# Optimization experiments

Measured on AMD Instinct MI355X. Metric: run time of the kernel, lower is better.

## Reference

```python
import jax, jax.numpy as jnp
import numpy as np

H = W = 32
CROP = int(H * 0.8)  # 25, matches int(H*crop_ratio) in torch
MEAN = jnp.array([0.5071, 0.4867, 0.4408], jnp.float32).reshape(1, 3, 1, 1)
STD = jnp.array([0.2675, 0.2565, 0.2761], jnp.float32).reshape(1, 3, 1, 1)


def _bilinear(img, iy, ix):
    # img [C,H,W]; iy/ix [H,W] float pixel coords (reflected+clamped already)
    y0 = jnp.floor(iy); x0 = jnp.floor(ix)
    wy = iy - y0; wx = ix - x0
    y0i = jnp.clip(y0.astype(jnp.int32), 0, H - 1); y1i = jnp.clip(y0i + 1, 0, H - 1)
    x0i = jnp.clip(x0.astype(jnp.int32), 0, W - 1); x1i = jnp.clip(x0i + 1, 0, W - 1)
    v00 = img[:, y0i, x0i]; v01 = img[:, y0i, x1i]
    v10 = img[:, y1i, x0i]; v11 = img[:, y1i, x1i]
    return v00 * (1 - wy) * (1 - wx) + v01 * (1 - wy) * wx + v10 * wy * (1 - wx) + v11 * wy * wx


def _reflect(c, size):
    # PyTorch grid_sample reflection padding, align_corners=False (reflect about -0.5 / size-0.5)
    lo = -0.5
    span = float(size)
    t = jnp.abs(c - lo)
    extra = jnp.mod(t, span)
    flips = jnp.floor(t / span)
    out = jnp.where(jnp.mod(flips, 2.0) == 0.0, lo + extra, lo + span - extra)
    return jnp.clip(out, 0.0, size - 1.0)


def _crop_resize_one(img, top, left):
    # bilinear resize of img[:, top:top+CROP, left:left+CROP] -> HxW, align_corners=False
    d = (jnp.arange(W, dtype=jnp.float32) + 0.5) * (CROP / W) - 0.5
    d = jnp.maximum(d, 0.0)
    i0 = jnp.floor(d).astype(jnp.int32)
    lam = d - i0
    i1 = jnp.minimum(i0 + 1, CROP - 1)
    r0 = top + i0; r1 = top + i1; c0 = left + i0; c1 = left + i1
    v00 = img[:, r0[:, None], c0[None, :]]
    v01 = img[:, r0[:, None], c1[None, :]]
    v10 = img[:, r1[:, None], c0[None, :]]
    v11 = img[:, r1[:, None], c1[None, :]]
    ly = lam[:, None]; lx = lam[None, :]
    return v00 * (1 - ly) * (1 - lx) + v01 * (1 - ly) * lx + v10 * ly * (1 - lx) + v11 * ly * lx


def _grid_sample_one(img, theta):
    # affine_grid + grid_sample (bilinear, reflection, align_corners=False)
    xs = (2.0 * (jnp.arange(W, dtype=jnp.float32) + 0.5) / W) - 1.0
    ys = (2.0 * (jnp.arange(H, dtype=jnp.float32) + 0.5) / H) - 1.0
    yn, xn = jnp.meshgrid(ys, xs, indexing='ij')
    gx = theta[0, 0] * xn + theta[0, 1] * yn + theta[0, 2]
    gy = theta[1, 0] * xn + theta[1, 1] * yn + theta[1, 2]
    ix = _reflect(((gx + 1.0) * W - 1.0) * 0.5, W)
    iy = _reflect(((gy + 1.0) * H - 1.0) * 0.5, H)
    return _bilinear(img, iy, ix)


def _augment(x, shared_affine, apply_crop):
    B = x.shape[0]
    ks = jax.random.split(jax.random.key(42), 10)
    x = x * STD + MEAN  # de-normalize
    if apply_crop:
        max_off = H - CROP
        top = jax.random.randint(ks[0], (B,), 0, max_off + 1)
        left = jax.random.randint(ks[1], (B,), 0, max_off + 1)
        x = jax.vmap(_crop_resize_one)(x, top, left)
    flip_mask = jax.random.uniform(ks[2], (B,)) < 0.5
    x = jnp.where(flip_mask[:, None, None, None], x[..., ::-1], x)
    # shared affine is provided -> always applied (torch shared_affine branch)
    x = jax.vmap(_grid_sample_one)(x, shared_affine)
    brightness = 1.0 + (jax.random.uniform(ks[3], (B, 1, 1, 1)) - 0.5) * 0.8
    x = x * brightness
    gray = x.mean(axis=1, keepdims=True)
    contrast = 1.0 + (jax.random.uniform(ks[4], (B, 1, 1, 1)) - 0.5) * 0.8
    x = gray + (x - gray) * contrast
    gray = x.mean(axis=1, keepdims=True)
    saturation = 1.0 + (jax.random.uniform(ks[5], (B, 1, 1, 1)) - 0.5) * 0.8
    x = gray + (x - gray) * saturation
    hue_mask = jax.random.uniform(ks[6], (B,)) < 0.5
    x = jnp.where(hue_mask[:, None, None, None], x[:, ::-1], x)  # BGR swap
    gray_mask = jax.random.uniform(ks[7], (B,)) < 0.2
    x = jnp.where(gray_mask[:, None, None, None], x.mean(axis=1, keepdims=True), x)
    blur_mask = jax.random.uniform(ks[8], (B,)) < 0.5
    xp = jnp.pad(x, ((0, 0), (0, 0), (1, 1), (1, 1)), mode='edge')  # replicate pad
    bl = sum(xp[:, :, i:i + H, j:j + W] for i in range(3) for j in range(3)) / 9.0  # 3x3 box blur
    x = jnp.where(blur_mask[:, None, None, None], bl, x)
    solar_mask = jax.random.uniform(ks[9], (B,)) < 0.1
    x = jnp.where(solar_mask[:, None, None, None] & (x > 0.5), 1.0 - x, x)
    x = jnp.clip(x, 0.0, 1.0)
    x = (x - MEAN) / STD  # re-normalize
    return x, flip_mask


def setup_inputs() -> dict:
    key = jax.random.key(0)
    k1, k2 = jax.random.split(key)
    B = 8192
    x = jax.random.normal(k1, (B, 3, H, W), jnp.float32)
    eye = jnp.broadcast_to(jnp.array([[1.0, 0.0, 0.0], [0.0, 1.0, 0.0]], jnp.float32), (B, 2, 3))
    shared_affine = eye + 0.1 * jax.random.normal(k2, (B, 2, 3), jnp.float32)
    return {"x": x, "shared_affine": shared_affine, "apply_crop": 1}


def reference(x, shared_affine, apply_crop):
    out, flip_mask = _augment(x, shared_affine, int(apply_crop))
    # torch returns (x, {'flip': flip_mask, 'affine': affine_theta})
    return out, flip_mask, shared_affine
```

## Files before the change

### kernel.cpp

```cpp
#include <hip/hip_runtime.h>

#define HW 32
#define NPIX 1024
#define IMG 3072

__device__ __forceinline__ unsigned rotl32(unsigned x, int d) {
    return (x << d) | (x >> (32 - d));
}

struct UPair { unsigned a, b; };

__device__ __forceinline__ UPair threefry2x32(unsigned k0, unsigned k1,
                                              unsigned x0, unsigned x1) {
    unsigned k2 = k0 ^ k1 ^ 0x1BD11BDAu;
    x0 += k0; x1 += k1;
#define RND(r) { x0 += x1; x1 = rotl32(x1, (r)); x1 ^= x0; }
    RND(13) RND(15) RND(26) RND(6)
    x0 += k1; x1 += k2 + 1u;
    RND(17) RND(29) RND(16) RND(24)
    x0 += k2; x1 += k0 + 2u;
    RND(13) RND(15) RND(26) RND(6)
    x0 += k0; x1 += k1 + 3u;
    RND(17) RND(29) RND(16) RND(24)
    x0 += k1; x1 += k2 + 4u;
    RND(13) RND(15) RND(26) RND(6)
    x0 += k2; x1 += k0 + 5u;
#undef RND
    return {x0, x1};
}

__device__ __forceinline__ float bits_to_u01(unsigned bits) {
    return __uint_as_float((bits >> 9) | 0x3f800000u) - 1.0f;
}

__device__ __forceinline__ float reflect32(float c) {
    float t = fabsf(c + 0.5f);
    float flips = floorf(t * 0.03125f);
    float extra = fmaf(flips, -32.0f, t);
    float o = (((int)flips) & 1) ? (31.5f - extra) : (extra - 0.5f);
    return fminf(fmaxf(o, 0.0f), 31.0f);
}

__global__ __launch_bounds__(256) void aug_kernel(
    const float* __restrict__ xin, const float* __restrict__ aff,
    const int* __restrict__ apply_crop, float* __restrict__ out, int B) {
    __shared__ __align__(16) float bufA[IMG];
    __shared__ __align__(16) float bufB[IMG];
    __shared__ float s_theta[6];
    __shared__ int s_j0[32];
    __shared__ float s_fr[32];
    __shared__ int s_top, s_left, s_flip, s_hue, s_gray, s_blur, s_solar;
    __shared__ float s_bright, s_contr, s_sat;

    const int b = blockIdx.x;
    const int t = threadIdx.x;
    const bool do_crop = (apply_crop[0] != 0);

    const float MEANc[3] = {0.5071f, 0.4867f, 0.4408f};
    const float STDc[3]  = {0.2675f, 0.2565f, 0.2761f};
    const float INVSTD[3] = {1.0f / 0.2675f, 1.0f / 0.2565f, 1.0f / 0.2761f};

    const float4* imgv = (const float4*)(xin + (size_t)b * IMG);
    float4 ld0 = imgv[t];
    float4 ld1 = imgv[t + 256];
    float4 ld2 = imgv[t + 512];

    const size_t OUT_IMG = (size_t)B * IMG;
    if (t < 6) {
        float v = aff[b * 6 + t];
        s_theta[t] = v;
        out[OUT_IMG + (size_t)B + (size_t)b * 6 + t] = v;
    }

    if (t < 32) {
        float d = fmaxf(((float)t + 0.5f) * 0.78125f - 0.5f, 0.0f);
        int j0 = (int)d;
        s_j0[t] = j0;
        s_fr[t] = d - (float)j0;
    }

    if (t < 10) {
        int k = t;
        UPair K = threefry2x32(0u, 42u, 0u, (unsigned)k);
        if (k < 2) {
            UPair k2 = threefry2x32(K.a, K.b, 0u, 1u);
            UPair r = threefry2x32(k2.a, k2.b, 0u, (unsigned)b);
            int val = (int)((r.a ^ r.b) & 7u);
            if (k == 0) s_top = val; else s_left = val;
        } else {
            UPair r = threefry2x32(K.a, K.b, 0u, (unsigned)b);
            float u = bits_to_u01(r.a ^ r.b);
            if      (k == 2) s_flip  = (u < 0.5f);
            else if (k == 3) s_bright = 1.0f + (u - 0.5f) * 0.8f;
            else if (k == 4) s_contr  = 1.0f + (u - 0.5f) * 0.8f;
            else if (k == 5) s_sat    = 1.0f + (u - 0.5f) * 0.8f;
            else if (k == 6) s_hue   = (u < 0.5f);
            else if (k == 7) s_gray  = (u < 0.2f);
            else if (k == 8) s_blur  = (u < 0.5f);
            else             s_solar = (u < 0.1f);
        }
    }

    {
        float4 v = ld0;
        v.x = v.x * STDc[0] + MEANc[0]; v.y = v.y * STDc[0] + MEANc[0];
        v.z = v.z * STDc[0] + MEANc[0]; v.w = v.w * STDc[0] + MEANc[0];
        ((float4*)bufA)[t] = v;
        v = ld1;
        v.x = v.x * STDc[1] + MEANc[1]; v.y = v.y * STDc[1] + MEANc[1];
        v.z = v.z * STDc[1] + MEANc[1]; v.w = v.w * STDc[1] + MEANc[1];
        ((float4*)bufA)[t + 256] = v;
        v = ld2;
        v.x = v.x * STDc[2] + MEANc[2]; v.y = v.y * STDc[2] + MEANc[2];
        v.z = v.z * STDc[2] + MEANc[2]; v.w = v.w * STDc[2] + MEANc[2];
        ((float4*)bufA)[t + 512] = v;
    }
    __syncthreads();

    if (t == 0) out[OUT_IMG + b] = s_flip ? 1.0f : 0.0f;

    float* cur = bufA;
    float* nxt = bufB;

    if (do_crop) {
        const int top = s_top, left = s_left;
#pragma unroll
        for (int m = 0; m < 4; ++m) {
            int s = t + 256 * m;
            int yi = s >> 5, xj = s & 31;
            int i0 = s_j0[yi]; float ly = s_fr[yi];
            int q0 = s_j0[xj]; float lx = s_fr[xj];
            int i1 = min(i0 + 1, 24);
            int q1 = min(q0 + 1, 24);
            int r0 = (top + i0) << 5, r1 = (top + i1) << 5;
            int c0 = left + q0, c1 = left + q1;
            float omy = 1.0f - ly, omx = 1.0f - lx;
            float w00 = omy * omx, w01 = omy * lx;
            float w10 = ly * omx, w11 = ly * lx;
            int a00 = r0 + c0, a01 = r0 + c1, a10 = r1 + c0, a11 = r1 + c1;
#pragma unroll
            for (int c = 0; c < 3; ++c) {
                const float* p = cur + c * NPIX;
                nxt[c * NPIX + s] = fmaf(p[a00], w00, fmaf(p[a01], w01,
                                    fmaf(p[a10], w10, p[a11] * w11)));
            }
        }
        float* tp = cur; cur = nxt; nxt = tp;
        __syncthreads();
    }

    {
        const int flip = s_flip, hue = s_hue, grayf = s_gray;
        const float br = s_bright;
        const float ctsa = s_contr * s_sat;
        const float th0 = s_theta[0], th1 = s_theta[1], th2 = s_theta[2];
        const float th3 = s_theta[3], th4 = s_theta[4], th5 = s_theta[5];
#pragma unroll
        for (int m = 0; m < 4; ++m) {
            int s = t + 256 * m;
            int yi = s >> 5, xj = s & 31;
            float xn = (float)xj * 0.0625f - 0.96875f;
            float yn = (float)yi * 0.0625f - 0.96875f;
            float gx = fmaf(th0, xn, fmaf(th1, yn, th2));
            float gy = fmaf(th3, xn, fmaf(th4, yn, th5));
            float ix = reflect32(fmaf(gx, 16.0f, 15.5f));
            float iy = reflect32(fmaf(gy, 16.0f, 15.5f));
            float fy = floorf(iy), fx = floorf(ix);
            float wy = iy - fy, wx = ix - fx;
            int y0 = (int)fy; int y1 = min(y0 + 1, 31);
            int x0 = (int)fx; int x1 = min(x0 + 1, 31);
            if (flip) { x0 = 31 - x0; x1 = 31 - x1; }
            int r0 = y0 << 5, r1 = y1 << 5;
            float omy = 1.0f - wy, omx = 1.0f - wx;
            float w00 = omy * omx, w01 = omy * wx;
            float w10 = wy * omx, w11 = wy * wx;
            int a00 = r0 + x0, a01 = r0 + x1, a10 = r1 + x0, a11 = r1 + x1;
            float ch0, ch1, ch2;
            {
                const float* p = cur;
                ch0 = fmaf(p[a00], w00, fmaf(p[a01], w01,
                       fmaf(p[a10], w10, p[a11] * w11)));
            }
            {
                const float* p = cur + NPIX;
                ch1 = fmaf(p[a00], w00, fmaf(p[a01], w01,
                       fmaf(p[a10], w10, p[a11] * w11)));
            }
            {
                const float* p = cur + 2 * NPIX;
                ch2 = fmaf(p[a00], w00, fmaf(p[a01], w01,
                       fmaf(p[a10], w10, p[a11] * w11)));
            }
            ch0 *= br; ch1 *= br; ch2 *= br;
            float g = (ch0 + ch1 + ch2) * (1.0f / 3.0f);
            ch0 = fmaf(ch0 - g, ctsa, g);
            ch1 = fmaf(ch1 - g, ctsa, g);
            ch2 = fmaf(ch2 - g, ctsa, g);
            if (hue) { float tmp = ch0; ch0 = ch2; ch2 = tmp; }
            if (grayf) { ch0 = ch1 = ch2 = g; }
            nxt[s] = ch0; nxt[NPIX + s] = ch1; nxt[2 * NPIX + s] = ch2;
        }
        float* tp = cur; cur = nxt; nxt = tp;
        __syncthreads();
    }

    const int blur = s_blur, solar = s_solar;

    if (blur) {
#pragma unroll
        for (int m = 0; m < 4; ++m) {
            int s = t + 256 * m;
            int yi = s >> 5, xj = s & 31;
            int yc = yi << 5;
            int xm = max(xj - 1, 0), xp = min(xj + 1, 31);
#pragma unroll
            for (int c = 0; c < 3; ++c) {
                const float* p = cur + c * NPIX;
                nxt[c * NPIX + s] = p[yc + xm] + p[yc + xj] + p[yc + xp];
            }
        }
        __syncthreads();
    }

    {
        float* o = out + (size_t)b * IMG;
#pragma unroll
        for (int m = 0; m < 4; ++m) {
            int s = t + 256 * m;
            int yi = s >> 5, xj = s & 31;
            int ym = max(yi - 1, 0) << 5, yp = min(yi + 1, 31) << 5;
#pragma unroll
            for (int c = 0; c < 3; ++c) {
                float r;
                if (blur) {
                    const float* h = nxt + c * NPIX;
                    r = (h[ym + xj] + h[s] + h[yp + xj]) * (1.0f / 9.0f);
                } else {
                    r = cur[c * NPIX + s];
                }
                if (solar && r > 0.5f) r = 1.0f - r;
                r = fminf(fmaxf(r, 0.0f), 1.0f);
                r = (r - MEANc[c]) * INVSTD[c];
                o[c * NPIX + s] = r;
            }
        }
    }
}

extern "C" void kernel_launch(void* const* d_in, const int* in_sizes, int n_in,
                              void* d_out, int out_size, void* d_ws, size_t ws_size,
                              hipStream_t stream) {
    const float* x = (const float*)d_in[0];
    const float* aff = (const float*)d_in[1];
    const int* ac = (const int*)d_in[2];
    float* out = (float*)d_out;
    int B = in_sizes[0] / IMG;
    aug_kernel<<<dim3(B), dim3(256), 0, stream>>>(x, aff, ac, out, B);
}
```

Before: 181.7 us.

## Process each image with one wavefront using interleaved RGB LDS and register pipeline

The kernel now uses one 64-thread wavefront per image instead of 256 threads. Each lane keeps 16 pixels in registers across stages. Shared memory holds a single interleaved RGBx float4 buffer, so each bilinear tap is one vector LDS read, and the double buffer and all block barriers are gone. The horizontal blur uses cross-lane shuffles, per-image parameters are made wave-uniform with readfirstlane, and output stores are float4. The trade-off is fewer waves per CU, which means less latency hiding, and higher register pressure.

```diff
diff --git a/kernel.cpp b/kernel.cpp
--- a/kernel.cpp
+++ b/kernel.cpp
@@ -3,6 +3,8 @@
 #define HW 32
 #define NPIX 1024
 #define IMG 3072
+
+typedef float vf4 __attribute__((ext_vector_type(4)));
 
 __device__ __forceinline__ unsigned rotl32(unsigned x, int d) {
     return (x << d) | (x >> (32 - d));
@@ -41,14 +43,18 @@
     return fminf(fmaxf(o, 0.0f), 31.0f);
 }
 
-__global__ __launch_bounds__(256) void aug_kernel(
+__device__ __forceinline__ float rfl_f(float v) {
+    return __uint_as_float(__builtin_amdgcn_readfirstlane(__float_as_uint(v)));
+}
+__device__ __forceinline__ int rfl_i(int v) {
+    return __builtin_amdgcn_readfirstlane(v);
+}
+
+__global__ __launch_bounds__(64) void aug_kernel(
     const float* __restrict__ xin, const float* __restrict__ aff,
     const int* __restrict__ apply_crop, float* __restrict__ out, int B) {
-    __shared__ __align__(16) float bufA[IMG];
-    __shared__ __align__(16) float bufB[IMG];
+    __shared__ vf4 buf[NPIX];
     __shared__ float s_theta[6];
-    __shared__ int s_j0[32];
-    __shared__ float s_fr[32];
     __shared__ int s_top, s_left, s_flip, s_hue, s_gray, s_blur, s_solar;
     __shared__ float s_bright, s_contr, s_sat;
 
@@ -56,27 +62,21 @@
     const int t = threadIdx.x;
     const bool do_crop = (apply_crop[0] != 0);
 
-    const float MEANc[3] = {0.5071f, 0.4867f, 0.4408f};
-    const float STDc[3]  = {0.2675f, 0.2565f, 0.2761f};
-    const float INVSTD[3] = {1.0f / 0.2675f, 1.0f / 0.2565f, 1.0f / 0.2761f};
-
-    const float4* imgv = (const float4*)(xin + (size_t)b * IMG);
-    float4 ld0 = imgv[t];
-    float4 ld1 = imgv[t + 256];
-    float4 ld2 = imgv[t + 512];
+    const float* src = xin + (size_t)b * IMG;
+    vf4 L0[4], L1[4], L2[4];
+#pragma unroll
+    for (int m = 0; m < 4; ++m) {
+        int p = 256 * m + 4 * t;
+        L0[m] = *(const vf4*)(src + p);
+        L1[m] = *(const vf4*)(src + NPIX + p);
+        L2[m] = *(const vf4*)(src + 2 * NPIX + p);
+    }
 
     const size_t OUT_IMG = (size_t)B * IMG;
     if (t < 6) {
         float v = aff[b * 6 + t];
         s_theta[t] = v;
         out[OUT_IMG + (size_t)B + (size_t)b * 6 + t] = v;
-    }
-
-    if (t < 32) {
-        float d = fmaxf(((float)t + 0.5f) * 0.78125f - 0.5f, 0.0f);
-        int j0 = (int)d;
-        s_j0[t] = j0;
-        s_fr[t] = d - (float)j0;
     }
 
     if (t < 10) {
@@ -101,64 +101,74 @@
         }
     }
 
-    {
-        float4 v = ld0;
-        v.x = v.x * STDc[0] + MEANc[0]; v.y = v.y * STDc[0] + MEANc[0];
-        v.z = v.z * STDc[0] + MEANc[0]; v.w = v.w * STDc[0] + MEANc[0];
-        ((float4*)bufA)[t] = v;
-        v = ld1;
-        v.x = v.x * STDc[1] + MEANc[1]; v.y = v.y * STDc[1] + MEANc[1];
-        v.z = v.z * STDc[1] + MEANc[1]; v.w = v.w * STDc[1] + MEANc[1];
-        ((float4*)bufA)[t + 256] = v;
-        v = ld2;
-        v.x = v.x * STDc[2] + MEANc[2]; v.y = v.y * STDc[2] + MEANc[2];
-        v.z = v.z * STDc[2] + MEANc[2]; v.w = v.w * STDc[2] + MEANc[2];
-        ((float4*)bufA)[t + 512] = v;
-    }
-    __syncthreads();
+#pragma unroll
+    for (int m = 0; m < 4; ++m) {
+        int p = 256 * m + 4 * t;
+#pragma unroll
+        for (int j = 0; j < 4; ++j) {
+            vf4 v;
+            v.x = fmaf(L0[m][j], 0.2675f, 0.5071f);
+            v.y = fmaf(L1[m][j], 0.2565f, 0.4867f);
+            v.z = fmaf(L2[m][j], 0.2761f, 0.4408f);
+            v.w = 0.0f;
+            buf[p + j] = v;
+        }
+    }
 
     if (t == 0) out[OUT_IMG + b] = s_flip ? 1.0f : 0.0f;
-
-    float* cur = bufA;
-    float* nxt = bufB;
+    const int top  = rfl_i(s_top),  left = rfl_i(s_left);
+    const int flip = rfl_i(s_flip), hue  = rfl_i(s_hue);
+    const int gray = rfl_i(s_gray), blur = rfl_i(s_blur), solar = rfl_i(s_solar);
+    const float br   = rfl_f(s_bright);
+    const float ctsa = rfl_f(s_contr) * rfl_f(s_sat);
+    const float th0 = rfl_f(s_theta[0]), th1 = rfl_f(s_theta[1]), th2 = rfl_f(s_theta[2]);
+    const float th3 = rfl_f(s_theta[3]), th4 = rfl_f(s_theta[4]), th5 = rfl_f(s_theta[5]);
+
+    float cx[16], cy[16], cz[16];
 
     if (do_crop) {
-        const int top = s_top, left = s_left;
-#pragma unroll
-        for (int m = 0; m < 4; ++m) {
-            int s = t + 256 * m;
-            int yi = s >> 5, xj = s & 31;
-            int i0 = s_j0[yi]; float ly = s_fr[yi];
-            int q0 = s_j0[xj]; float lx = s_fr[xj];
-            int i1 = min(i0 + 1, 24);
-            int q1 = min(q0 + 1, 24);
-            int r0 = (top + i0) << 5, r1 = (top + i1) << 5;
-            int c0 = left + q0, c1 = left + q1;
-            float omy = 1.0f - ly, omx = 1.0f - lx;
-            float w00 = omy * omx, w01 = omy * lx;
-            float w10 = ly * omx, w11 = ly * lx;
-            int a00 = r0 + c0, a01 = r0 + c1, a10 = r1 + c0, a11 = r1 + c1;
-#pragma unroll
-            for (int c = 0; c < 3; ++c) {
-                const float* p = cur + c * NPIX;
-                nxt[c * NPIX + s] = fmaf(p[a00], w00, fmaf(p[a01], w01,
-                                    fmaf(p[a10], w10, p[a11] * w11)));
-            }
-        }
-        float* tp = cur; cur = nxt; nxt = tp;
-        __syncthreads();
-    }
-
-    {
-        const int flip = s_flip, hue = s_hue, grayf = s_gray;
-        const float br = s_bright;
-        const float ctsa = s_contr * s_sat;
-        const float th0 = s_theta[0], th1 = s_theta[1], th2 = s_theta[2];
-        const float th3 = s_theta[3], th4 = s_theta[4], th5 = s_theta[5];
-#pragma unroll
-        for (int m = 0; m < 4; ++m) {
-            int s = t + 256 * m;
-            int yi = s >> 5, xj = s & 31;
+#pragma unroll
+        for (int m = 0; m < 4; ++m) {
+#pragma unroll
+            for (int j = 0; j < 4; ++j) {
+                const int i = 4 * m + j;
+                int p = 256 * m + 4 * t + j;
+                int yi = p >> 5, xj = p & 31;
+                float dy = fmaxf(fmaf((float)yi, 0.78125f, -0.109375f), 0.0f);
+                int i0 = (int)dy; float ly = dy - (float)i0; int i1 = min(i0 + 1, 24);
+                float dx = fmaxf(fmaf((float)xj, 0.78125f, -0.109375f), 0.0f);
+                int q0 = (int)dx; float lx = dx - (float)q0; int q1 = min(q0 + 1, 24);
+                int r0 = (top + i0) << 5, r1 = (top + i1) << 5;
+                int c0 = left + q0, c1 = left + q1;
+                float omy = 1.0f - ly, omx = 1.0f - lx;
+                float w00 = omy * omx, w01 = omy * lx;
+                float w10 = ly * omx, w11 = ly * lx;
+                vf4 t00 = buf[r0 + c0], t01 = buf[r0 + c1];
+                vf4 t10 = buf[r1 + c0], t11 = buf[r1 + c1];
+                cx[i] = fmaf(t00.x, w00, fmaf(t01.x, w01, fmaf(t10.x, w10, t11.x * w11)));
+                cy[i] = fmaf(t00.y, w00, fmaf(t01.y, w01, fmaf(t10.y, w10, t11.y * w11)));
+                cz[i] = fmaf(t00.z, w00, fmaf(t01.z, w01, fmaf(t10.z, w10, t11.z * w11)));
+            }
+        }
+#pragma unroll
+        for (int m = 0; m < 4; ++m) {
+#pragma unroll
+            for (int j = 0; j < 4; ++j) {
+                const int i = 4 * m + j;
+                int p = 256 * m + 4 * t + j;
+                vf4 v; v.x = cx[i]; v.y = cy[i]; v.z = cz[i]; v.w = 0.0f;
+                buf[p] = v;
+            }
+        }
+    }
+
+#pragma unroll
+    for (int m = 0; m < 4; ++m) {
+#pragma unroll
+        for (int j = 0; j < 4; ++j) {
+            const int i = 4 * m + j;
+            int p = 256 * m + 4 * t + j;
+            int yi = p >> 5, xj = p & 31;
             float xn = (float)xj * 0.0625f - 0.96875f;
             float yn = (float)yi * 0.0625f - 0.96875f;
             float gx = fmaf(th0, xn, fmaf(th1, yn, th2));
@@ -174,75 +184,102 @@
             float omy = 1.0f - wy, omx = 1.0f - wx;
             float w00 = omy * omx, w01 = omy * wx;
             float w10 = wy * omx, w11 = wy * wx;
-            int a00 = r0 + x0, a01 = r0 + x1, a10 = r1 + x0, a11 = r1 + x1;
-            float ch0, ch1, ch2;
-            {
-                const float* p = cur;
-                ch0 = fmaf(p[a00], w00, fmaf(p[a01], w01,
-                       fmaf(p[a10], w10, p[a11] * w11)));
-            }
-            {
-                const float* p = cur + NPIX;
-                ch1 = fmaf(p[a00], w00, fmaf(p[a01], w01,
-                       fmaf(p[a10], w10, p[a11] * w11)));
-            }
-            {
-                const float* p = cur + 2 * NPIX;
-                ch2 = fmaf(p[a00], w00, fmaf(p[a01], w01,
-                       fmaf(p[a10], w10, p[a11] * w11)));
-            }
+            vf4 t00 = buf[r0 + x0], t01 = buf[r0 + x1];
+            vf4 t10 = buf[r1 + x0], t11 = buf[r1 + x1];
+            float ch0 = fmaf(t00.x, w00, fmaf(t01.x, w01, fmaf(t10.x, w10, t11.x * w11)));
+            float ch1 = fmaf(t00.y, w00, fmaf(t01.y, w01, fmaf(t10.y, w10, t11.y * w11)));
+            float ch2 = fmaf(t00.z, w00, fmaf(t01.z, w01, fmaf(t10.z, w10, t11.z * w11)));
             ch0 *= br; ch1 *= br; ch2 *= br;
             float g = (ch0 + ch1 + ch2) * (1.0f / 3.0f);
             ch0 = fmaf(ch0 - g, ctsa, g);
             ch1 = fmaf(ch1 - g, ctsa, g);
             ch2 = fmaf(ch2 - g, ctsa, g);
             if (hue) { float tmp = ch0; ch0 = ch2; ch2 = tmp; }
-            if (grayf) { ch0 = ch1 = ch2 = g; }
-            nxt[s] = ch0; nxt[NPIX + s] = ch1; nxt[2 * NPIX + s] = ch2;
-        }
-        float* tp = cur; cur = nxt; nxt = tp;
-        __syncthreads();
-    }
-
-    const int blur = s_blur, solar = s_solar;
+            if (gray) { ch0 = ch1 = ch2 = g; }
+            cx[i] = ch0; cy[i] = ch1; cz[i] = ch2;
+        }
+    }
 
     if (blur) {
-#pragma unroll
-        for (int m = 0; m < 4; ++m) {
-            int s = t + 256 * m;
-            int yi = s >> 5, xj = s & 31;
-            int yc = yi << 5;
-            int xm = max(xj - 1, 0), xp = min(xj + 1, 31);
-#pragma unroll
-            for (int c = 0; c < 3; ++c) {
-                const float* p = cur + c * NPIX;
-                nxt[c * NPIX + s] = p[yc + xm] + p[yc + xj] + p[yc + xp];
-            }
-        }
-        __syncthreads();
+        const int le = ((t & 7) == 0), re = ((t & 7) == 7);
+        const int tl = (t - 1) & 63, tr = (t + 1) & 63;
+#pragma unroll
+        for (int m = 0; m < 4; ++m) {
+            const int q = 4 * m;
+            {
+                float v0 = cx[q], v1 = cx[q+1], v2 = cx[q+2], v3 = cx[q+3];
+                float lf = __shfl(v3, tl), rt = __shfl(v0, tr);
+                if (le) lf = v0;  if (re) rt = v3;
+                float s01 = v0 + v1, s23 = v2 + v3;
+                cx[q] = lf + s01; cx[q+1] = s01 + v2; cx[q+2] = v1 + s23; cx[q+3] = s23 + rt;
+            }
+            {
+                float v0 = cy[q], v1 = cy[q+1], v2 = cy[q+2], v3 = cy[q+3];
+                float lf = __shfl(v3, tl), rt = __shfl(v0, tr);
+                if (le) lf = v0;  if (re) rt = v3;
+                float s01 = v0 + v1, s23 = v2 + v3;
+                cy[q] = lf + s01; cy[q+1] = s01 + v2; cy[q+2] = v1 + s23; cy[q+3] = s23 + rt;
+            }
+            {
+                float v0 = cz[q], v1 = cz[q+1], v2 = cz[q+2], v3 = cz[q+3];
+                float lf = __shfl(v3, tl), rt = __shfl(v0, tr);
+                if (le) lf = v0;  if (re) rt = v3;
+                float s01 = v0 + v1, s23 = v2 + v3;
+                cz[q] = lf + s01; cz[q+1] = s01 + v2; cz[q+2] = v1 + s23; cz[q+3] = s23 + rt;
+            }
+        }
+#pragma unroll
+        for (int m = 0; m < 4; ++m) {
+#pragma unroll
+            for (int j = 0; j < 4; ++j) {
+                const int i = 4 * m + j;
+                int p = 256 * m + 4 * t + j;
+                vf4 v; v.x = cx[i]; v.y = cy[i]; v.z = cz[i]; v.w = 0.0f;
+                buf[p] = v;
+            }
+        }
+#pragma unroll
+        for (int m = 0; m < 4; ++m) {
+#pragma unroll
+            for (int j = 0; j < 4; ++j) {
+                const int i = 4 * m + j;
+                int p = 256 * m + 4 * t + j;
+                int yi = p >> 5, xj = p & 31;
+                vf4 up = buf[(max(yi - 1, 0) << 5) + xj];
+                vf4 dn = buf[(min(yi + 1, 31) << 5) + xj];
+                cx[i] = (up.x + cx[i] + dn.x) * (1.0f / 9.0f);
+                cy[i] = (up.y + cy[i] + dn.y) * (1.0f / 9.0f);
+                cz[i] = (up.z + cz[i] + dn.z) * (1.0f / 9.0f);
+            }
+        }
     }
 
     {
+        const float INV0 = 1.0f / 0.2675f, INV1 = 1.0f / 0.2565f, INV2 = 1.0f / 0.2761f;
         float* o = out + (size_t)b * IMG;
 #pragma unroll
         for (int m = 0; m < 4; ++m) {
-            int s = t + 256 * m;
-            int yi = s >> 5, xj = s & 31;
-            int ym = max(yi - 1, 0) << 5, yp = min(yi + 1, 31) << 5;
-#pragma unroll
-            for (int c = 0; c < 3; ++c) {
-                float r;
-                if (blur) {
-                    const float* h = nxt + c * NPIX;
-                    r = (h[ym + xj] + h[s] + h[yp + xj]) * (1.0f / 9.0f);
-                } else {
-                    r = cur[c * NPIX + s];
+            int p = 256 * m + 4 * t;
+            vf4 o0, o1, o2;
+#pragma unroll
+            for (int j = 0; j < 4; ++j) {
+                const int i = 4 * m + j;
+                float r0v = cx[i], r1v = cy[i], r2v = cz[i];
+                if (solar) {
+                    if (r0v > 0.5f) r0v = 1.0f - r0v;
+                    if (r1v > 0.5f) r1v = 1.0f - r1v;
+                    if (r2v > 0.5f) r2v = 1.0f - r2v;
                 }
-                if (solar && r > 0.5f) r = 1.0f - r;
-                r = fminf(fmaxf(r, 0.0f), 1.0f);
-                r = (r - MEANc[c]) * INVSTD[c];
-                o[c * NPIX + s] = r;
-            }
+                r0v = fminf(fmaxf(r0v, 0.0f), 1.0f);
+                r1v = fminf(fmaxf(r1v, 0.0f), 1.0f);
+                r2v = fminf(fmaxf(r2v, 0.0f), 1.0f);
+                o0[j] = (r0v - 0.5071f) * INV0;
+                o1[j] = (r1v - 0.4867f) * INV1;
+                o2[j] = (r2v - 0.4408f) * INV2;
+            }
+            *(vf4*)(o + p) = o0;
+            *(vf4*)(o + NPIX + p) = o1;
+            *(vf4*)(o + 2 * NPIX + p) = o2;
         }
     }
 }
@@ -255,5 +292,5 @@
     const int* ac = (const int*)d_in[2];
     float* out = (float*)d_out;
     int B = in_sizes[0] / IMG;
-    aug_kernel<<<dim3(B), dim3(256), 0, stream>>>(x, aff, ac, out, B);
-}
+    aug_kernel<<<dim3(B), dim3(64), 0, stream>>>(x, aff, ac, out, B);
+}
```

New measurement: 195.1 us. +7.3%, slower.
